# Optimization experiments

Measured on AMD Instinct MI355X. Metric: run time of the kernel, lower is better.

Reference implementation:

```python
import jax, jax.numpy as jnp
import numpy as np

N_LEVELS = 16
FEAT = 2
LOG2_T = 19
T = 1 << LOG2_T
PER_LEVEL_SCALE = 1.5
BASE_RES = 16
SCALE = 1.0
N_FREQ = 3
HASH_PRIME = np.uint32(2654435761)


def _level_params(level):
    # tcnn HashGrid: scale = 2^(level*log2(pls)) * base_res - 1; res = ceil(scale)+1
    scale = float(2.0 ** (level * np.log2(PER_LEVEL_SCALE)) * BASE_RES - 1.0)
    res = int(np.ceil(scale)) + 1
    return scale, res


def hash_encode(xy, tables):
    # xy: [N,2] in [0,1]; tables: [N_LEVELS, T, FEAT]
    outs = []
    for l in range(N_LEVELS):
        scale, res = _level_params(l)
        pos = xy * scale + 0.5
        pos_f = jnp.floor(pos)
        frac = pos - pos_f              # [N,2]
        pi = pos_f.astype(jnp.int32)    # [N,2]
        dense = (res * res) <= T

        def idx(ix, iy):
            if dense:
                return ix + iy * res
            h = ix.astype(jnp.uint32) ^ (iy.astype(jnp.uint32) * HASH_PRIME)
            return (h % np.uint32(T)).astype(jnp.int32)

        ix, iy = pi[:, 0], pi[:, 1]
        tbl = tables[l]
        f00 = tbl[idx(ix, iy)]
        f10 = tbl[idx(ix + 1, iy)]
        f01 = tbl[idx(ix, iy + 1)]
        f11 = tbl[idx(ix + 1, iy + 1)]
        wx = frac[:, 0:1]
        wy = frac[:, 1:2]
        outs.append((f00 * (1 - wx) + f10 * wx) * (1 - wy)
                    + (f01 * (1 - wx) + f11 * wx) * wy)
    return jnp.concatenate(outs, axis=-1)  # [N, 32]


def prior_net(xy, Wp1, Wp2, Wp3):
    # tcnn Frequency encoding (3 freqs, sin+cos per dim) + bias-free sigmoid MLP
    freqs = (2.0 ** jnp.arange(N_FREQ, dtype=jnp.float32)) * jnp.pi
    ang = xy[:, :, None] * freqs  # [N,2,3]
    enc = jnp.concatenate([jnp.sin(ang), jnp.cos(ang)], axis=-1).reshape(xy.shape[0], -1)  # [N,12]
    h = jax.nn.sigmoid(enc @ Wp1)
    h = jax.nn.sigmoid(h @ Wp2)
    return h @ Wp3  # [N,1]


def setup_inputs() -> dict:
    key = jax.random.key(0)
    ks = jax.random.split(key, 7)
    N = 2_000_000
    inputs = jax.random.normal(ks[0], (N, 3), dtype=jnp.float32)
    # tcnn-style small init for hash table entries
    hash_tables = jax.random.uniform(ks[1], (N_LEVELS, T, FEAT), dtype=jnp.float32,
                                     minval=-1e-4, maxval=1e-4)
    in_dim = N_LEVELS * FEAT  # 32
    W_tiny = jax.random.normal(ks[2], (in_dim, 65), dtype=jnp.float32) / np.sqrt(in_dim)
    b_tiny = jnp.zeros((65,), dtype=jnp.float32)
    Wp1 = jax.random.normal(ks[3], (2 * 2 * N_FREQ, 64), dtype=jnp.float32) / np.sqrt(12.0)
    Wp2 = jax.random.normal(ks[4], (64, 64), dtype=jnp.float32) / 8.0
    Wp3 = jax.random.normal(ks[5], (64, 1), dtype=jnp.float32) / 8.0
    return {"inputs": inputs, "hash_tables": hash_tables, "W_tiny": W_tiny,
            "b_tiny": b_tiny, "Wp1": Wp1, "Wp2": Wp2, "Wp3": Wp3}


def reference(inputs, hash_tables, W_tiny, b_tiny, Wp1, Wp2, Wp3):
    # forward_core(inputs, 0, output_height=False, delta=True, gradient=False)
    prior_z = jax.lax.stop_gradient(prior_net(inputs[:, :2], Wp1, Wp2, Wp3))  # detached
    z_vals = inputs[:, 2:]           # taken BEFORE scaling, as in torch code
    xin = inputs * SCALE
    feat = hash_encode(xin[:, :2] / 30.0 + 0.5, hash_tables)
    x = feat @ W_tiny + b_tiny       # [N,65]
    return jnp.concatenate([z_vals - x[:, :1] / SCALE - prior_z, x[:, 1:]], axis=-1)
```

## Files before the change

kernel.cpp:

```cpp
#include <hip/hip_runtime.h>

#define TSZ (1u << 19)
#define HPRIME 2654435761u

typedef short bf16x8 __attribute__((ext_vector_type(8)));
typedef float f32x4 __attribute__((ext_vector_type(4)));

__device__ __forceinline__ float sigmoidf(float x) {
    return 1.0f / (1.0f + __expf(-x));
}

__device__ __forceinline__ unsigned short f2b(float f) {
    union { float f; unsigned u; } v; v.f = f;
    return (unsigned short)((v.u + 0x7FFFu + ((v.u >> 16) & 1u)) >> 16);
}

__device__ __forceinline__ unsigned f2b_pack(float a, float b) {
    union { float f; unsigned u; } x, y; x.f = a; y.f = b;
    unsigned ra = (x.u + 0x7FFFu + ((x.u >> 16) & 1u)) >> 16;
    unsigned rb = (y.u + 0x7FFFu + ((y.u >> 16) & 1u)) & 0xFFFF0000u;
    return ra | rb;
}

__global__ void repack_frags(const float* __restrict__ Wp2,
                             const float* __restrict__ Wt,
                             unsigned short* __restrict__ wp2F,
                             unsigned short* __restrict__ wtF) {
    int t = blockIdx.x * blockDim.x + threadIdx.x;
    if (t < 4096) {
        int j = t & 7, lane = (t >> 3) & 63, f = t >> 9;
        int ks = f >> 2, nt = f & 3;
        int k = ks * 32 + (lane >> 4) * 8 + j;
        int n = nt * 16 + (lane & 15);
        wp2F[t] = f2b(Wp2[k * 64 + n]);
    }
    if (t < 2048) {
        int j = t & 7, lane = (t >> 3) & 63, nt = t >> 9;
        int k = (lane >> 4) * 8 + j;
        int n = nt * 16 + (lane & 15);
        wtF[t] = f2b(Wt[k * 65 + 1 + n]);
    }
}

__global__ __launch_bounds__(256, 4)
void sdf_main(const float* __restrict__ in,
              const float* __restrict__ tables,
              const float* __restrict__ Wp1,
              const float* __restrict__ Wp3,
              const float* __restrict__ bt,
              const float* __restrict__ Wt,
              const unsigned short* __restrict__ wp2F,
              const unsigned short* __restrict__ wtF,
              float* __restrict__ out, int N)
{
    __shared__ unsigned short Abuf[4 * 64 * 72];
    __shared__ float sPrior[256];

    const int tid = threadIdx.x;
    const int wave = tid >> 6, lane = tid & 63;
    const int quad = lane >> 4, col = lane & 15;
    const long long n0 = (long long)blockIdx.x * 256;
    const int n = (int)n0 + tid;
    const int nc = n < N ? n : N - 1;

    const float px = in[nc * 3 + 0];
    const float py = in[nc * 3 + 1];
    const float pz = in[nc * 3 + 2];

    const float PIF = 3.14159274101257324e+00f;
    float e[12];
    e[0] = __sinf(px * PIF); e[1]  = __sinf(px * (2.0f * PIF)); e[2]  = __sinf(px * (4.0f * PIF));
    e[3] = __cosf(px * PIF); e[4]  = __cosf(px * (2.0f * PIF)); e[5]  = __cosf(px * (4.0f * PIF));
    e[6] = __sinf(py * PIF); e[7]  = __sinf(py * (2.0f * PIF)); e[8]  = __sinf(py * (4.0f * PIF));
    e[9] = __cosf(py * PIF); e[10] = __cosf(py * (2.0f * PIF)); e[11] = __cosf(py * (4.0f * PIF));

    unsigned short* myA = Abuf + wave * 64 * 72 + lane * 72;
#pragma unroll
    for (int j4 = 0; j4 < 64; j4 += 4) {
        float s0 = 0.f, s1 = 0.f, s2 = 0.f, s3 = 0.f;
#pragma unroll
        for (int k = 0; k < 12; k++) {
            const float4 w = *(const float4*)(Wp1 + k * 64 + j4);
            s0 += e[k] * w.x; s1 += e[k] * w.y; s2 += e[k] * w.z; s3 += e[k] * w.w;
        }
        uint2 pk;
        pk.x = f2b_pack(sigmoidf(s0), sigmoidf(s1));
        pk.y = f2b_pack(sigmoidf(s2), sigmoidf(s3));
        *reinterpret_cast<uint2*>(myA + j4) = pk;
    }

    bf16x8 bfr[8];
#pragma unroll
    for (int f = 0; f < 8; f++)
        bfr[f] = *reinterpret_cast<const bf16x8*>(wp2F + (f * 64 + lane) * 8);
    float w3[4];
#pragma unroll
    for (int nt = 0; nt < 4; nt++) w3[nt] = Wp3[nt * 16 + col];

#pragma unroll
    for (int mt = 0; mt < 4; mt++) {
        const unsigned short* ar = Abuf + wave * 4608 + (mt * 16 + col) * 72;
        const bf16x8 a0 = *reinterpret_cast<const bf16x8*>(ar + quad * 8);
        const bf16x8 a1 = *reinterpret_cast<const bf16x8*>(ar + 32 + quad * 8);
        float pp[4] = {0.f, 0.f, 0.f, 0.f};
#pragma unroll
        for (int nt = 0; nt < 4; nt++) {
            f32x4 acc = {0.f, 0.f, 0.f, 0.f};
            acc = __builtin_amdgcn_mfma_f32_16x16x32_bf16(a0, bfr[nt], acc, 0, 0, 0);
            acc = __builtin_amdgcn_mfma_f32_16x16x32_bf16(a1, bfr[4 + nt], acc, 0, 0, 0);
#pragma unroll
            for (int r = 0; r < 4; r++)
                pp[r] += w3[nt] * sigmoidf(acc[r]);
        }
#pragma unroll
        for (int r = 0; r < 4; r++) {
            pp[r] += __shfl_xor(pp[r], 1, 64);
            pp[r] += __shfl_xor(pp[r], 2, 64);
            pp[r] += __shfl_xor(pp[r], 4, 64);
            pp[r] += __shfl_xor(pp[r], 8, 64);
            if (col == r) sPrior[wave * 64 + mt * 16 + quad * 4 + r] = pp[r];
        }
    }

    const float scl[16] = {15.f, 23.f, 35.f, 53.f, 80.f, 120.5f, 181.25f, 272.375f,
                           409.0625f, 614.09375f, 921.640625f, 1382.9609375f,
                           2074.94140625f, 3112.912109375f, 4669.8681640625f,
                           7005.30224609375f};
    const int ress[10] = {16, 24, 36, 54, 81, 122, 183, 274, 411, 616};
    const float cx = __fadd_rn(__fdiv_rn(px, 30.0f), 0.5f);
    const float cy = __fadd_rn(__fdiv_rn(py, 30.0f), 0.5f);

    unsigned short* myF = Abuf + wave * 4608 + lane * 40;
    float x0 = bt[0];
    unsigned pk[4];
#pragma unroll
    for (int l = 0; l < 16; l++) {
        const float sc = scl[l];
        const float posx = __fadd_rn(__fmul_rn(cx, sc), 0.5f);
        const float posy = __fadd_rn(__fmul_rn(cy, sc), 0.5f);
        const float fx = floorf(posx), fy = floorf(posy);
        const float wx = __fsub_rn(posx, fx), wy = __fsub_rn(posy, fy);
        const int ix = (int)fx, iy = (int)fy;
        const float* tbl = tables + (size_t)l * (size_t)(TSZ * 2);
        int i00, i10, i01, i11;
        if (l < 10) {
            const int r = ress[l];
            i00 = ix + iy * r; i10 = i00 + 1; i01 = i00 + r; i11 = i01 + 1;
        } else {
            const unsigned ux = (unsigned)ix, uy = (unsigned)iy;
            const unsigned hy0 = uy * HPRIME, hy1 = (uy + 1u) * HPRIME;
            i00 = (int)((ux ^ hy0) & (TSZ - 1u));
            i10 = (int)(((ux + 1u) ^ hy0) & (TSZ - 1u));
            i01 = (int)((ux ^ hy1) & (TSZ - 1u));
            i11 = (int)(((ux + 1u) ^ hy1) & (TSZ - 1u));
        }
        const float2 q00 = *(const float2*)(tbl + 2 * i00);
        const float2 q10 = *(const float2*)(tbl + 2 * i10);
        const float2 q01 = *(const float2*)(tbl + 2 * i01);
        const float2 q11 = *(const float2*)(tbl + 2 * i11);
        const float omx = 1.0f - wx, omy = 1.0f - wy;
        const float f0 = (q00.x * omx + q10.x * wx) * omy + (q01.x * omx + q11.x * wx) * wy;
        const float f1 = (q00.y * omx + q10.y * wx) * omy + (q01.y * omx + q11.y * wx) * wy;
        x0 += f0 * Wt[(2 * l) * 65] + f1 * Wt[(2 * l + 1) * 65];
        pk[l & 3] = f2b_pack(f0, f1);
        if ((l & 3) == 3) {
            uint4 v; v.x = pk[0]; v.y = pk[1]; v.z = pk[2]; v.w = pk[3];
            *reinterpret_cast<uint4*>(myF + (l - 3) * 2) = v;
        }
    }

    const float priorMe = sPrior[wave * 64 + lane];

    {
        bf16x8 fa[4];
#pragma unroll
        for (int mt = 0; mt < 4; mt++)
            fa[mt] = *reinterpret_cast<const bf16x8*>(
                Abuf + wave * 4608 + (mt * 16 + col) * 40 + quad * 8);
        bf16x8 wb[4];
        float bb[4];
#pragma unroll
        for (int nt = 0; nt < 4; nt++) {
            wb[nt] = *reinterpret_cast<const bf16x8*>(wtF + (nt * 64 + lane) * 8);
            bb[nt] = bt[1 + nt * 16 + col];
        }
        const long long wbase = n0 + (long long)wave * 64;
        float* op = out + (size_t)wbase * 65;
        const bool full = (wbase + 64 <= (long long)N);
#pragma unroll
        for (int mt = 0; mt < 4; mt++) {
#pragma unroll
            for (int nt = 0; nt < 4; nt++) {
                f32x4 acc = {0.f, 0.f, 0.f, 0.f};
                acc = __builtin_amdgcn_mfma_f32_16x16x32_bf16(fa[mt], wb[nt], acc, 0, 0, 0);
                if (full) {
#pragma unroll
                    for (int r = 0; r < 4; r++)
                        op[(mt * 16 + quad * 4 + r) * 65 + 1 + nt * 16 + col] = acc[r] + bb[nt];
                } else {
#pragma unroll
                    for (int r = 0; r < 4; r++) {
                        const int row = mt * 16 + quad * 4 + r;
                        if (wbase + row < (long long)N)
                            op[(size_t)row * 65 + 1 + nt * 16 + col] = acc[r] + bb[nt];
                    }
                }
            }
        }
        if (n < N) out[(size_t)n * 65] = pz - x0 - priorMe;
    }
}

extern "C" void kernel_launch(void* const* d_in, const int* in_sizes, int n_in,
                              void* d_out, int out_size, void* d_ws, size_t ws_size,
                              hipStream_t stream) {
    const float* inputs = (const float*)d_in[0];
    const float* tables = (const float*)d_in[1];
    const float* W_tiny = (const float*)d_in[2];
    const float* b_tiny = (const float*)d_in[3];
    const float* Wp1    = (const float*)d_in[4];
    const float* Wp2    = (const float*)d_in[5];
    const float* Wp3    = (const float*)d_in[6];
    float* out = (float*)d_out;
    unsigned short* wp2F = (unsigned short*)d_ws;
    unsigned short* wtF  = wp2F + 4096;

    const int N = in_sizes[0] / 3;

    hipLaunchKernelGGL(repack_frags, dim3(16), dim3(256), 0, stream,
                       Wp2, W_tiny, wp2F, wtF);

    const int grid = (N + 255) / 256;
    hipLaunchKernelGGL(sdf_main, dim3(grid), dim3(256), 0, stream,
                       inputs, tables, Wp1, Wp3, b_tiny, W_tiny, wp2F, wtF, out, N);
}
```

Before: 919.3 us.

## Move prior-net first layer to MFMA, swizzle LDS, batch hash-grid gathers

Replaces the scalar FP32 12x64 first prior layer with a bf16 MFMA, using a K dimension zero-padded to 32 and weights repacked once in the setup kernel. The LDS buffer shrinks to 64 columns per row with an XOR swizzle to avoid bank conflicts, and the separate sPrior shared array is replaced by wave shuffles. Hash-grid lookups are grouped four levels at a time so more gathers are in flight at once, and occupancy is raised to 5 blocks per CU. This trades extra register pressure and bf16 rounding of the encoding inputs for fewer VALU FMAs and better memory latency hiding.

```diff
diff --git a/kernel.cpp b/kernel.cpp
--- a/kernel.cpp
+++ b/kernel.cpp
@@ -22,10 +22,16 @@
     return ra | rb;
 }
 
+__device__ __forceinline__ int swz(int row, int s) {
+    return (row << 6) + ((((s >> 3) ^ (row & 7)) << 3) | (s & 7));
+}
+
 __global__ void repack_frags(const float* __restrict__ Wp2,
                              const float* __restrict__ Wt,
+                             const float* __restrict__ Wp1,
                              unsigned short* __restrict__ wp2F,
-                             unsigned short* __restrict__ wtF) {
+                             unsigned short* __restrict__ wtF,
+                             unsigned short* __restrict__ wp1F) {
     int t = blockIdx.x * blockDim.x + threadIdx.x;
     if (t < 4096) {
         int j = t & 7, lane = (t >> 3) & 63, f = t >> 9;
@@ -39,22 +45,22 @@
         int k = (lane >> 4) * 8 + j;
         int n = nt * 16 + (lane & 15);
         wtF[t] = f2b(Wt[k * 65 + 1 + n]);
-    }
-}
-
-__global__ __launch_bounds__(256, 4)
+        wp1F[t] = (k < 12) ? f2b(Wp1[k * 64 + n]) : (unsigned short)0;
+    }
+}
+
+__global__ __launch_bounds__(256, 5)
 void sdf_main(const float* __restrict__ in,
               const float* __restrict__ tables,
-              const float* __restrict__ Wp1,
               const float* __restrict__ Wp3,
               const float* __restrict__ bt,
               const float* __restrict__ Wt,
               const unsigned short* __restrict__ wp2F,
               const unsigned short* __restrict__ wtF,
+              const unsigned short* __restrict__ wp1F,
               float* __restrict__ out, int N)
 {
-    __shared__ unsigned short Abuf[4 * 64 * 72];
-    __shared__ float sPrior[256];
+    __shared__ __align__(16) unsigned short Abuf[4 * 64 * 64];
 
     const int tid = threadIdx.x;
     const int wave = tid >> 6, lane = tid & 63;
@@ -67,6 +73,8 @@
     const float py = in[nc * 3 + 1];
     const float pz = in[nc * 3 + 2];
 
+    unsigned short* WB = Abuf + (wave << 12);
+
     const float PIF = 3.14159274101257324e+00f;
     float e[12];
     e[0] = __sinf(px * PIF); e[1]  = __sinf(px * (2.0f * PIF)); e[2]  = __sinf(px * (4.0f * PIF));
@@ -74,51 +82,81 @@
     e[6] = __sinf(py * PIF); e[7]  = __sinf(py * (2.0f * PIF)); e[8]  = __sinf(py * (4.0f * PIF));
     e[9] = __cosf(py * PIF); e[10] = __cosf(py * (2.0f * PIF)); e[11] = __cosf(py * (4.0f * PIF));
 
-    unsigned short* myA = Abuf + wave * 64 * 72 + lane * 72;
-#pragma unroll
-    for (int j4 = 0; j4 < 64; j4 += 4) {
-        float s0 = 0.f, s1 = 0.f, s2 = 0.f, s3 = 0.f;
-#pragma unroll
-        for (int k = 0; k < 12; k++) {
-            const float4 w = *(const float4*)(Wp1 + k * 64 + j4);
-            s0 += e[k] * w.x; s1 += e[k] * w.y; s2 += e[k] * w.z; s3 += e[k] * w.w;
-        }
-        uint2 pk;
-        pk.x = f2b_pack(sigmoidf(s0), sigmoidf(s1));
-        pk.y = f2b_pack(sigmoidf(s2), sigmoidf(s3));
-        *reinterpret_cast<uint2*>(myA + j4) = pk;
-    }
-
-    bf16x8 bfr[8];
-#pragma unroll
-    for (int f = 0; f < 8; f++)
-        bfr[f] = *reinterpret_cast<const bf16x8*>(wp2F + (f * 64 + lane) * 8);
-    float w3[4];
-#pragma unroll
-    for (int nt = 0; nt < 4; nt++) w3[nt] = Wp3[nt * 16 + col];
-
-#pragma unroll
-    for (int mt = 0; mt < 4; mt++) {
-        const unsigned short* ar = Abuf + wave * 4608 + (mt * 16 + col) * 72;
-        const bf16x8 a0 = *reinterpret_cast<const bf16x8*>(ar + quad * 8);
-        const bf16x8 a1 = *reinterpret_cast<const bf16x8*>(ar + 32 + quad * 8);
-        float pp[4] = {0.f, 0.f, 0.f, 0.f};
-#pragma unroll
-        for (int nt = 0; nt < 4; nt++) {
-            f32x4 acc = {0.f, 0.f, 0.f, 0.f};
-            acc = __builtin_amdgcn_mfma_f32_16x16x32_bf16(a0, bfr[nt], acc, 0, 0, 0);
-            acc = __builtin_amdgcn_mfma_f32_16x16x32_bf16(a1, bfr[4 + nt], acc, 0, 0, 0);
-#pragma unroll
-            for (int r = 0; r < 4; r++)
-                pp[r] += w3[nt] * sigmoidf(acc[r]);
-        }
-#pragma unroll
-        for (int r = 0; r < 4; r++) {
-            pp[r] += __shfl_xor(pp[r], 1, 64);
-            pp[r] += __shfl_xor(pp[r], 2, 64);
-            pp[r] += __shfl_xor(pp[r], 4, 64);
-            pp[r] += __shfl_xor(pp[r], 8, 64);
-            if (col == r) sPrior[wave * 64 + mt * 16 + quad * 4 + r] = pp[r];
+    {
+        uint4 v0, v1, vz;
+        v0.x = f2b_pack(e[0], e[1]);  v0.y = f2b_pack(e[2], e[3]);
+        v0.z = f2b_pack(e[4], e[5]);  v0.w = f2b_pack(e[6], e[7]);
+        v1.x = f2b_pack(e[8], e[9]);  v1.y = f2b_pack(e[10], e[11]);
+        v1.z = 0u; v1.w = 0u;
+        vz.x = vz.y = vz.z = vz.w = 0u;
+        *reinterpret_cast<uint4*>(WB + swz(lane, 0))  = v0;
+        *reinterpret_cast<uint4*>(WB + swz(lane, 8))  = v1;
+        *reinterpret_cast<uint4*>(WB + swz(lane, 16)) = vz;
+        *reinterpret_cast<uint4*>(WB + swz(lane, 24)) = vz;
+    }
+
+    {
+        bf16x8 w1f[4];
+#pragma unroll
+        for (int nt = 0; nt < 4; nt++)
+            w1f[nt] = *reinterpret_cast<const bf16x8*>(wp1F + (nt * 64 + lane) * 8);
+#pragma unroll
+        for (int mt = 0; mt < 4; mt++) {
+            const bf16x8 ea = *reinterpret_cast<const bf16x8*>(WB + swz(mt * 16 + col, quad * 8));
+#pragma unroll
+            for (int nt = 0; nt < 4; nt++) {
+                f32x4 acc = {0.f, 0.f, 0.f, 0.f};
+                acc = __builtin_amdgcn_mfma_f32_16x16x32_bf16(ea, w1f[nt], acc, 0, 0, 0);
+#pragma unroll
+                for (int r = 0; r < 4; r++) {
+                    const int row = mt * 16 + quad * 4 + r;
+                    WB[swz(row, nt * 16 + col)] = f2b(sigmoidf(acc[r]));
+                }
+            }
+        }
+    }
+
+    float priorMe = 0.f;
+    {
+        bf16x8 bfr[8];
+#pragma unroll
+        for (int f = 0; f < 8; f++)
+            bfr[f] = *reinterpret_cast<const bf16x8*>(wp2F + (f * 64 + lane) * 8);
+        float w3[4];
+#pragma unroll
+        for (int nt = 0; nt < 4; nt++) w3[nt] = Wp3[nt * 16 + col];
+
+#pragma unroll
+        for (int mt = 0; mt < 4; mt++) {
+            const int arow = mt * 16 + col;
+            const bf16x8 a0 = *reinterpret_cast<const bf16x8*>(WB + swz(arow, quad * 8));
+            const bf16x8 a1 = *reinterpret_cast<const bf16x8*>(WB + swz(arow, 32 + quad * 8));
+            float pp[4] = {0.f, 0.f, 0.f, 0.f};
+#pragma unroll
+            for (int nt = 0; nt < 4; nt++) {
+                f32x4 acc = {0.f, 0.f, 0.f, 0.f};
+                acc = __builtin_amdgcn_mfma_f32_16x16x32_bf16(a0, bfr[nt], acc, 0, 0, 0);
+                acc = __builtin_amdgcn_mfma_f32_16x16x32_bf16(a1, bfr[4 + nt], acc, 0, 0, 0);
+#pragma unroll
+                for (int r = 0; r < 4; r++)
+                    pp[r] += w3[nt] * sigmoidf(acc[r]);
+            }
+#pragma unroll
+            for (int r = 0; r < 4; r++) {
+                pp[r] += __shfl_xor(pp[r], 1, 64);
+                pp[r] += __shfl_xor(pp[r], 2, 64);
+                pp[r] += __shfl_xor(pp[r], 4, 64);
+                pp[r] += __shfl_xor(pp[r], 8, 64);
+            }
+            const int src = ((lane >> 2) & 3) * 16;
+            const float t0 = __shfl(pp[0], src, 64);
+            const float t1 = __shfl(pp[1], src, 64);
+            const float t2 = __shfl(pp[2], src, 64);
+            const float t3 = __shfl(pp[3], src, 64);
+            const float ta = (lane & 1) ? t1 : t0;
+            const float tb = (lane & 1) ? t3 : t2;
+            const float sel = (lane & 2) ? tb : ta;
+            if ((lane >> 4) == mt) priorMe = sel;
         }
     }
 
@@ -130,53 +168,61 @@
     const float cx = __fadd_rn(__fdiv_rn(px, 30.0f), 0.5f);
     const float cy = __fadd_rn(__fdiv_rn(py, 30.0f), 0.5f);
 
-    unsigned short* myF = Abuf + wave * 4608 + lane * 40;
     float x0 = bt[0];
-    unsigned pk[4];
-#pragma unroll
-    for (int l = 0; l < 16; l++) {
-        const float sc = scl[l];
-        const float posx = __fadd_rn(__fmul_rn(cx, sc), 0.5f);
-        const float posy = __fadd_rn(__fmul_rn(cy, sc), 0.5f);
-        const float fx = floorf(posx), fy = floorf(posy);
-        const float wx = __fsub_rn(posx, fx), wy = __fsub_rn(posy, fy);
-        const int ix = (int)fx, iy = (int)fy;
-        const float* tbl = tables + (size_t)l * (size_t)(TSZ * 2);
-        int i00, i10, i01, i11;
-        if (l < 10) {
-            const int r = ress[l];
-            i00 = ix + iy * r; i10 = i00 + 1; i01 = i00 + r; i11 = i01 + 1;
-        } else {
-            const unsigned ux = (unsigned)ix, uy = (unsigned)iy;
-            const unsigned hy0 = uy * HPRIME, hy1 = (uy + 1u) * HPRIME;
-            i00 = (int)((ux ^ hy0) & (TSZ - 1u));
-            i10 = (int)(((ux + 1u) ^ hy0) & (TSZ - 1u));
-            i01 = (int)((ux ^ hy1) & (TSZ - 1u));
-            i11 = (int)(((ux + 1u) ^ hy1) & (TSZ - 1u));
-        }
-        const float2 q00 = *(const float2*)(tbl + 2 * i00);
-        const float2 q10 = *(const float2*)(tbl + 2 * i10);
-        const float2 q01 = *(const float2*)(tbl + 2 * i01);
-        const float2 q11 = *(const float2*)(tbl + 2 * i11);
-        const float omx = 1.0f - wx, omy = 1.0f - wy;
-        const float f0 = (q00.x * omx + q10.x * wx) * omy + (q01.x * omx + q11.x * wx) * wy;
-        const float f1 = (q00.y * omx + q10.y * wx) * omy + (q01.y * omx + q11.y * wx) * wy;
-        x0 += f0 * Wt[(2 * l) * 65] + f1 * Wt[(2 * l + 1) * 65];
-        pk[l & 3] = f2b_pack(f0, f1);
-        if ((l & 3) == 3) {
-            uint4 v; v.x = pk[0]; v.y = pk[1]; v.z = pk[2]; v.w = pk[3];
-            *reinterpret_cast<uint4*>(myF + (l - 3) * 2) = v;
-        }
-    }
-
-    const float priorMe = sPrior[wave * 64 + lane];
+#pragma unroll
+    for (int cc = 0; cc < 4; cc++) {
+        float2 q00[4], q10[4], q01[4], q11[4];
+        float wxa[4], wya[4];
+#pragma unroll
+        for (int u = 0; u < 4; u++) {
+            const int l = cc * 4 + u;
+            const float sc = scl[l];
+            const float posx = __fadd_rn(__fmul_rn(cx, sc), 0.5f);
+            const float posy = __fadd_rn(__fmul_rn(cy, sc), 0.5f);
+            const float fx = floorf(posx), fy = floorf(posy);
+            wxa[u] = __fsub_rn(posx, fx);
+            wya[u] = __fsub_rn(posy, fy);
+            const int ix = (int)fx, iy = (int)fy;
+            const float* tbl = tables + (size_t)l * (size_t)(TSZ * 2);
+            int i00, i10, i01, i11;
+            if (l < 10) {
+                const int r = ress[l];
+                i00 = ix + iy * r; i10 = i00 + 1; i01 = i00 + r; i11 = i01 + 1;
+            } else {
+                const unsigned ux = (unsigned)ix, uy = (unsigned)iy;
+                const unsigned hy0 = uy * HPRIME, hy1 = (uy + 1u) * HPRIME;
+                i00 = (int)((ux ^ hy0) & (TSZ - 1u));
+                i10 = (int)(((ux + 1u) ^ hy0) & (TSZ - 1u));
+                i01 = (int)((ux ^ hy1) & (TSZ - 1u));
+                i11 = (int)(((ux + 1u) ^ hy1) & (TSZ - 1u));
+            }
+            q00[u] = *(const float2*)(tbl + 2 * i00);
+            q10[u] = *(const float2*)(tbl + 2 * i10);
+            q01[u] = *(const float2*)(tbl + 2 * i01);
+            q11[u] = *(const float2*)(tbl + 2 * i11);
+        }
+        unsigned pk[4];
+#pragma unroll
+        for (int u = 0; u < 4; u++) {
+            const int l = cc * 4 + u;
+            const float wx = wxa[u], wy = wya[u];
+            const float omx = 1.0f - wx, omy = 1.0f - wy;
+            const float f0 = (q00[u].x * omx + q10[u].x * wx) * omy +
+                             (q01[u].x * omx + q11[u].x * wx) * wy;
+            const float f1 = (q00[u].y * omx + q10[u].y * wx) * omy +
+                             (q01[u].y * omx + q11[u].y * wx) * wy;
+            x0 += f0 * Wt[(2 * l) * 65] + f1 * Wt[(2 * l + 1) * 65];
+            pk[u] = f2b_pack(f0, f1);
+        }
+        uint4 v; v.x = pk[0]; v.y = pk[1]; v.z = pk[2]; v.w = pk[3];
+        *reinterpret_cast<uint4*>(WB + swz(lane, cc * 8)) = v;
+    }
 
     {
         bf16x8 fa[4];
 #pragma unroll
         for (int mt = 0; mt < 4; mt++)
-            fa[mt] = *reinterpret_cast<const bf16x8*>(
-                Abuf + wave * 4608 + (mt * 16 + col) * 40 + quad * 8);
+            fa[mt] = *reinterpret_cast<const bf16x8*>(WB + swz(mt * 16 + col, quad * 8));
         bf16x8 wb[4];
         float bb[4];
 #pragma unroll
@@ -224,13 +270,14 @@
     float* out = (float*)d_out;
     unsigned short* wp2F = (unsigned short*)d_ws;
     unsigned short* wtF  = wp2F + 4096;
+    unsigned short* wp1F = wtF + 2048;
 
     const int N = in_sizes[0] / 3;
 
     hipLaunchKernelGGL(repack_frags, dim3(16), dim3(256), 0, stream,
-                       Wp2, W_tiny, wp2F, wtF);
+                       Wp2, W_tiny, Wp1, wp2F, wtF, wp1F);
 
     const int grid = (N + 255) / 256;
     hipLaunchKernelGGL(sdf_main, dim3(grid), dim3(256), 0, stream,
-                       inputs, tables, Wp1, Wp3, b_tiny, W_tiny, wp2F, wtF, out, N);
-}
+                       inputs, tables, Wp3, b_tiny, W_tiny, wp2F, wtF, wp1F, out, N);
+}
```

Result: slower. 982.9 us (+6.9%).
